# Performance work log

Hardware: AMD Instinct MI355X
Metric: run time of the kernel (lower is better)

## Reference

```python
import jax, jax.numpy as jnp
import numpy as np

B, CIN, COUT, HID, L, H, W = 4, 3, 1, 128, 4, 256, 256


def setup_inputs() -> dict:
    key = jax.random.key(0)
    ks = jax.random.split(key, 12)
    u = 1.0 / (HID * HID)
    inp = {
        "x": jax.random.normal(ks[0], (B, CIN, H, W), dtype=jnp.float32),
        "lin_in_w": jax.random.normal(ks[1], (CIN, HID), dtype=jnp.float32) * 0.1,
        "lin_in_b": jnp.zeros((HID,), dtype=jnp.float32),
        "wr": jax.random.uniform(ks[2], (L, HID, HID), dtype=jnp.float32) * u,
        "wi": jax.random.uniform(ks[3], (L, HID, HID), dtype=jnp.float32) * u,
        "br": jax.random.normal(ks[4], (L, HID), dtype=jnp.float32) * 0.01,
        "bi": jax.random.normal(ks[5], (L, HID), dtype=jnp.float32) * 0.01,
        "cw": jax.random.normal(ks[6], (L, HID, HID), dtype=jnp.float32) * (1.0 / np.sqrt(HID)),
        "cb": jnp.zeros((L, HID), dtype=jnp.float32),
        "lin_out_w": jax.random.normal(ks[7], (HID, COUT), dtype=jnp.float32) * 0.1,
        "lin_out_b": jnp.zeros((COUT,), dtype=jnp.float32),
    }
    return inp


def _gelu(x):
    return jax.nn.gelu(x, approximate=False)  # torch F.gelu default = exact erf


def _spectral_conv(x, wr, wi, br, bi):
    # x: (B, C, H, W) -> rfft2 over last two dims, per-frequency channel mix
    sp = jnp.fft.rfft2(x, axes=(-2, -1))  # (B, C, H, W//2+1) complex
    re = jnp.einsum('bixy,io->boxy', sp.real, wr) + br[None, :, None, None]
    im = jnp.einsum('bixy,io->boxy', sp.imag, wi) + bi[None, :, None, None]
    return jnp.fft.irfft2(re + 1j * im, s=x.shape[-2:], axes=(-2, -1))


def reference(x, lin_in_w, lin_in_b, wr, wi, br, bi, cw, cb, lin_out_w, lin_out_b):
    # input transform: BCHW -> BHWC -> Linear -> gelu -> BCHW
    h = jnp.einsum('bchw,cd->bdhw', x, lin_in_w) + lin_in_b[None, :, None, None]
    h = _gelu(h)
    for l in range(L):
        spatial = jnp.einsum('bihw,oi->bohw', h, cw[l]) + cb[l][None, :, None, None]  # 1x1 conv
        h = _gelu(spatial + _spectral_conv(h, wr[l], wi[l], br[l], bi[l]))
    # output transform
    y = jnp.einsum('bchw,cd->bdhw', h, lin_out_w) + lin_out_b[None, :, None, None]
    return _gelu(y)
```

## Files before the change

### kernel.cpp

```cpp
#include <hip/hip_runtime.h>

#define W2_FLOATS   131072
#define RB_FLOATS   131072
#define WBF_USHORTS 262144

typedef short s8v __attribute__((ext_vector_type(8)));
typedef float f4v __attribute__((ext_vector_type(4)));
typedef float f2v __attribute__((ext_vector_type(2)));

#if defined(__has_builtin)
#  if __has_builtin(__builtin_amdgcn_cvt_pk_bf16_f32)
#    define HAVE_PK_BF16 1
#  endif
#endif
#ifndef HAVE_PK_BF16
#  define HAVE_PK_BF16 0
#endif

__device__ __forceinline__ unsigned short bf16_rne(float v) {
    unsigned u = __float_as_uint(v);
    unsigned r = u + 0x7FFFu + ((u >> 16) & 1u);
    return (unsigned short)(r >> 16);
}
__device__ __forceinline__ float bf16_tof(unsigned short x) {
    return __uint_as_float(((unsigned)x) << 16);
}
__device__ __forceinline__ unsigned pk_bf16(float a, float b) {
#if HAVE_PK_BF16
    typedef __bf16 bf16x2 __attribute__((ext_vector_type(2)));
    bf16x2 v = __builtin_amdgcn_cvt_pk_bf16_f32(a, b);
    return __builtin_bit_cast(unsigned, v);
#else
    return (unsigned)bf16_rne(a) | ((unsigned)bf16_rne(b) << 16);
#endif
}

__device__ __forceinline__ float gelu_f(float x) {
    float ax = fabsf(x);
    float z  = ax * 0.7071067811865476f;
    float t  = __builtin_amdgcn_rcpf(fmaf(0.3275911f, z, 1.0f));
    float p  = t * fmaf(t, fmaf(t, fmaf(t, fmaf(t, 1.061405429f, -1.453152027f),
                                        1.421413741f), -0.284496736f), 0.254829592f);
    float e  = __expf(-z * z);
    float hx = 0.5f * ax;
    return fmaf(0.5f, x, hx) - hx * p * e;
}
__device__ __forceinline__ f2v gelu2(f2v x) {
    f2v ax; ax.x = fabsf(x.x); ax.y = fabsf(x.y);
    f2v z   = ax * 0.7071067811865476f;
    f2v den = z * 0.3275911f + 1.0f;
    f2v t;  t.x = __builtin_amdgcn_rcpf(den.x); t.y = __builtin_amdgcn_rcpf(den.y);
    f2v p = t * (t * (t * (t * (t * 1.061405429f + (-1.453152027f)) + 1.421413741f)
              + (-0.284496736f)) + 0.254829592f);
    f2v nz2 = -z * z;
    f2v e;  e.x = __expf(nz2.x); e.y = __expf(nz2.y);
    f2v hx = ax * 0.5f;
    return (x * 0.5f + hx) - (hx * p) * e;
}

__global__ void prep_all(const float* __restrict__ wr, const float* __restrict__ wi,
                         const float* __restrict__ cw,
                         const float* __restrict__ br, const float* __restrict__ bi,
                         float* __restrict__ W2, unsigned short* __restrict__ Wbf,
                         float* __restrict__ RB) {
    int bid = blockIdx.x;
    if (bid < 512) {
        int idx = bid * 256 + threadIdx.x;
        {
            int l = idx >> 15, which = (idx >> 14) & 1, i = (idx >> 7) & 127, o = idx & 127;
            const float* w = which ? wi : wr;
            W2[idx] = 0.5f * (cw[(l << 14) + (o << 7) + i] + w[(l << 14) + (i << 7) + o]);
        }
        {
            int t = idx;
            int j = t & 7, col = (t >> 3) & 127, quad = (t >> 10) & 3;
            int m2 = (t >> 12) & 1, kc = (t >> 13) & 3, l = t >> 15;
            int k = kc * 32 + quad * 8 + j;
            const float* w = m2 ? wi : wr;
            float v = 0.5f * (cw[(l << 14) + (col << 7) + k] + w[(l << 14) + (k << 7) + col]);
            unsigned short hi = bf16_rne(v);
            unsigned short lo = bf16_rne(v - bf16_tof(hi));
            int base = (l * 4 + kc) * 16384;
            Wbf[base + (((m2 * 2 + 0) * 4 + quad) * 128 + col) * 8 + j] = hi;
            Wbf[base + (((m2 * 2 + 1) * 4 + quad) * 128 + col) * 8 + j] = lo;
        }
    } else {
        int idx = (bid - 512) * 256 + threadIdx.x;
        int l = idx >> 15, c = (idx >> 7) & 255, o = idx & 127;
        float v;
        if (c == 0) {
            v = br[(l << 7) + o];
        } else {
            float s = 0.0f;
            for (int k = 1; k < 128; k++) {
                int m = (k * c) & 255;
                s += sinf(0.024543692952156857f * (float)m);
            }
            v = -bi[(l << 7) + o] * s * 0.0078125f;
        }
        RB[idx] = v;
    }
}

#define APAD 40
#define A_IDX(sd, kt, hf, pair, qj) ((((((sd)*4 + (kt))*2 + (hf))*32 + (pair))*APAD) + (qj))
#define W_IDX(m2, hf, quad, col) (((((m2)*2 + (hf))*4 + (quad))*128 + (col))*8)

__device__ __forceinline__ void layer_core(const unsigned short* Abuf,
        const unsigned short* __restrict__ Wl, int wv, int l15, int quad,
        f4v U[2], f4v V[2])
{
    U[0] = (f4v){0.f, 0.f, 0.f, 0.f}; U[1] = (f4v){0.f, 0.f, 0.f, 0.f};
    V[0] = (f4v){0.f, 0.f, 0.f, 0.f}; V[1] = (f4v){0.f, 0.f, 0.f, 0.f};
    #pragma unroll
    for (int kc = 0; kc < 4; kc++) {
        {
            s8v b0 = *(const s8v*)&Wl[kc * 16384 + W_IDX(0, 0, quad, wv * 16 + l15)];
            s8v b1 = *(const s8v*)&Wl[kc * 16384 + W_IDX(0, 1, quad, wv * 16 + l15)];
            s8v ah0 = *(const s8v*)&Abuf[A_IDX(0, kc, 0, l15,      quad * 8)];
            s8v ah1 = *(const s8v*)&Abuf[A_IDX(0, kc, 0, 16 + l15, quad * 8)];
            s8v al0 = *(const s8v*)&Abuf[A_IDX(0, kc, 1, l15,      quad * 8)];
            s8v al1 = *(const s8v*)&Abuf[A_IDX(0, kc, 1, 16 + l15, quad * 8)];
            U[0] = __builtin_amdgcn_mfma_f32_16x16x32_bf16(ah0, b0, U[0], 0, 0, 0);
            U[1] = __builtin_amdgcn_mfma_f32_16x16x32_bf16(ah1, b0, U[1], 0, 0, 0);
            U[0] = __builtin_amdgcn_mfma_f32_16x16x32_bf16(ah0, b1, U[0], 0, 0, 0);
            U[1] = __builtin_amdgcn_mfma_f32_16x16x32_bf16(ah1, b1, U[1], 0, 0, 0);
            U[0] = __builtin_amdgcn_mfma_f32_16x16x32_bf16(al0, b0, U[0], 0, 0, 0);
            U[1] = __builtin_amdgcn_mfma_f32_16x16x32_bf16(al1, b0, U[1], 0, 0, 0);
        }
        {
            s8v b0 = *(const s8v*)&Wl[kc * 16384 + W_IDX(1, 0, quad, wv * 16 + l15)];
            s8v b1 = *(const s8v*)&Wl[kc * 16384 + W_IDX(1, 1, quad, wv * 16 + l15)];
            s8v ah0 = *(const s8v*)&Abuf[A_IDX(1, kc, 0, l15,      quad * 8)];
            s8v ah1 = *(const s8v*)&Abuf[A_IDX(1, kc, 0, 16 + l15, quad * 8)];
            s8v al0 = *(const s8v*)&Abuf[A_IDX(1, kc, 1, l15,      quad * 8)];
            s8v al1 = *(const s8v*)&Abuf[A_IDX(1, kc, 1, 16 + l15, quad * 8)];
            V[0] = __builtin_amdgcn_mfma_f32_16x16x32_bf16(ah0, b0, V[0], 0, 0, 0);
            V[1] = __builtin_amdgcn_mfma_f32_16x16x32_bf16(ah1, b0, V[1], 0, 0, 0);
            V[0] = __builtin_amdgcn_mfma_f32_16x16x32_bf16(ah0, b1, V[0], 0, 0, 0);
            V[1] = __builtin_amdgcn_mfma_f32_16x16x32_bf16(ah1, b1, V[1], 0, 0, 0);
            V[0] = __builtin_amdgcn_mfma_f32_16x16x32_bf16(al0, b0, V[0], 0, 0, 0);
            V[1] = __builtin_amdgcn_mfma_f32_16x16x32_bf16(al1, b0, V[1], 0, 0, 0);
        }
    }
}

__global__ __launch_bounds__(512, 6) void fno_fused(
        const float* __restrict__ x,
        const float* __restrict__ w_in, const float* __restrict__ b_in,
        const unsigned short* __restrict__ Wbf,
        const float* __restrict__ W2,
        const float* __restrict__ RB,
        const float* __restrict__ cb,
        const float* __restrict__ wo, const float* __restrict__ bo,
        float* __restrict__ out)
{
    __shared__ unsigned short Abuf[2 * 4 * 2 * 32 * APAD];

    int bid = blockIdx.x;
    int tid = threadIdx.x;

    if (bid >= 4096) {
        float* Hs = (float*)Abuf;
        int b2 = bid - 4096;
        int o = tid & 127;
        int rowp = (tid < 128) ? 0 : 128;
        float hval = 0.0f;
        if (tid < 256) {
            float acc = b_in[o];
            #pragma unroll
            for (int c = 0; c < 3; c++)
                acc = fmaf(x[((b2 * 3 + c) << 16) + (rowp << 8)], w_in[c * 128 + o], acc);
            hval = gelu_f(acc);
        }
        for (int l = 0; l < 4; l++) {
            __syncthreads();
            if (tid < 256) Hs[tid] = hval;
            __syncthreads();
            if (tid < 256) {
                const float* W2l = W2 + l * 32768;
                const float* hb = Hs + ((tid < 128) ? 0 : 128);
                float a2 = 0.0f;
                for (int i = 0; i < 128; i++) a2 = fmaf(W2l[(i << 7) + o], hb[i], a2);
                a2 = 2.0f * a2 + cb[l * 128 + o];
                if (tid < 128) a2 += RB[l * 32768 + o];
                hval = gelu_f(a2);
            }
        }
        __syncthreads();
        if (tid < 256) Hs[tid] = hval * wo[o];
        __syncthreads();
        #pragma unroll
        for (int off = 64; off >= 1; off >>= 1) {
            if (tid < 256 && (tid & 127) < off) Hs[tid] += Hs[tid + off];
            __syncthreads();
        }
        if (tid < 256 && (tid & 127) == 0) out[(b2 << 16) + (rowp << 8)] = gelu_f(Hs[tid] + bo[0]);
        return;
    }

    int b = bid >> 10;
    int rem = bid & 1023;
    int r, c0, rq;
    bool rowzero;
    if (rem < 1016) {
        r = 1 + (rem >> 3);
        c0 = (rem & 7) << 5;
        rq = 256 - r;
        rowzero = false;
    } else {
        int idx2 = rem - 1016;
        r = (idx2 < 4) ? 0 : 128;
        c0 = 1 + ((idx2 & 3) << 5);
        rq = r;
        rowzero = (r == 0);
    }

    {
        int j2 = tid >> 4;
        int seg = tid & 15;
        int ch0 = seg << 3;
        int cp = c0 + j2;
        int cq = (256 - cp) & 255;
        float xp[3], xq[3];
        #pragma unroll
        for (int c = 0; c < 3; c++) {
            xp[c] = x[((b * 3 + c) << 16) + (r << 8) + cp];
            xq[c] = x[((b * 3 + c) << 16) + (rq << 8) + cq];
        }
        int kt = seg >> 2;
        int qj = (seg & 3) << 3;
        alignas(16) unsigned short sh[8], sl[8], dh[8], dl[8];
        #pragma unroll
        for (int jj = 0; jj < 8; jj++) {
            int d = ch0 + jj;
            float bv = b_in[d];
            f2v acc2; acc2.x = bv; acc2.y = bv;
            #pragma unroll
            for (int c = 0; c < 3; c++) {
                float w = w_in[c * 128 + d];
                f2v xv; xv.x = xp[c]; xv.y = xq[c];
                acc2 = xv * w + acc2;
            }
            f2v g = gelu2(acc2);
            float s = g.x + g.y, dd = g.x - g.y;
            unsigned hpk = pk_bf16(s, dd);
            f2v res;
            res.x = s  - __uint_as_float(hpk << 16);
            res.y = dd - __uint_as_float(hpk & 0xFFFF0000u);
            unsigned lpk = pk_bf16(res.x, res.y);
            sh[jj] = (unsigned short)hpk; dh[jj] = (unsigned short)(hpk >> 16);
            sl[jj] = (unsigned short)lpk; dl[jj] = (unsigned short)(lpk >> 16);
        }
        *(s8v*)&Abuf[A_IDX(0, kt, 0, j2, qj)] = *(const s8v*)sh;
        *(s8v*)&Abuf[A_IDX(0, kt, 1, j2, qj)] = *(const s8v*)sl;
        *(s8v*)&Abuf[A_IDX(1, kt, 0, j2, qj)] = *(const s8v*)dh;
        *(s8v*)&Abuf[A_IDX(1, kt, 1, j2, qj)] = *(const s8v*)dl;
    }

    int lane = tid & 63;
    int wv = tid >> 6;
    int l15 = lane & 15;
    int quad = lane >> 4;
    int och = wv * 16 + l15;
    int rkt = wv >> 1;
    int rqj = ((wv & 1) << 4) + l15;

    for (int l = 0; l < 3; l++) {
        __syncthreads();
        f4v U[2], V[2];
        layer_core(Abuf, Wbf + l * 65536, wv, l15, quad, U, V);
        __syncthreads();

        const float* RBl = RB + l * 32768;
        float cbv = cb[l * 128 + och];
        #pragma unroll
        for (int mt = 0; mt < 2; mt++)
            #pragma unroll
            for (int rg = 0; rg < 4; rg++) {
                int pair = mt * 16 + quad * 4 + rg;
                int colp = c0 + pair;
                int colq = (256 - colp) & 255;
                float u = U[mt][rg], v = V[mt][rg];
                f2v bpq; bpq.x = u + v + cbv; bpq.y = u - v + cbv;
                if (rowzero) {
                    bpq.x += RBl[(colp << 7) + och];
                    bpq.y += RBl[(colq << 7) + och];
                }
                f2v g = gelu2(bpq);
                float s = g.x + g.y, dd = g.x - g.y;
                unsigned hpk = pk_bf16(s, dd);
                f2v res;
                res.x = s  - __uint_as_float(hpk << 16);
                res.y = dd - __uint_as_float(hpk & 0xFFFF0000u);
                unsigned lpk = pk_bf16(res.x, res.y);
                Abuf[A_IDX(0, rkt, 0, pair, rqj)] = (unsigned short)hpk;
                Abuf[A_IDX(1, rkt, 0, pair, rqj)] = (unsigned short)(hpk >> 16);
                Abuf[A_IDX(0, rkt, 1, pair, rqj)] = (unsigned short)lpk;
                Abuf[A_IDX(1, rkt, 1, pair, rqj)] = (unsigned short)(lpk >> 16);
            }
    }

    float pp[8], pq[8];
    {
        __syncthreads();
        f4v U[2], V[2];
        layer_core(Abuf, Wbf + 3 * 65536, wv, l15, quad, U, V);
        __syncthreads();

        float wov = wo[och];
        const float* RBl = RB + 3 * 32768;
        float cbv = cb[3 * 128 + och];
        #pragma unroll
        for (int mt = 0; mt < 2; mt++)
            #pragma unroll
            for (int rg = 0; rg < 4; rg++) {
                int pair = mt * 16 + quad * 4 + rg;
                int colp = c0 + pair;
                int colq = (256 - colp) & 255;
                float u = U[mt][rg], v = V[mt][rg];
                f2v bpq; bpq.x = u + v + cbv; bpq.y = u - v + cbv;
                if (rowzero) {
                    bpq.x += RBl[(colp << 7) + och];
                    bpq.y += RBl[(colq << 7) + och];
                }
                f2v g = gelu2(bpq);
                pp[mt * 4 + rg] = g.x * wov;
                pq[mt * 4 + rg] = g.y * wov;
            }
    }

    #pragma unroll
    for (int i = 0; i < 8; i++) {
        #pragma unroll
        for (int m = 1; m <= 8; m <<= 1) {
            pp[i] += __shfl_xor(pp[i], m, 64);
            pq[i] += __shfl_xor(pq[i], m, 64);
        }
    }
    float* Pb = (float*)Abuf;
    if (l15 == 0) {
        #pragma unroll
        for (int mt = 0; mt < 2; mt++)
            #pragma unroll
            for (int rg = 0; rg < 4; rg++) {
                int pair = mt * 16 + quad * 4 + rg;
                Pb[(pair << 3) + wv]        = pp[mt * 4 + rg];
                Pb[256 + (pair << 3) + wv]  = pq[mt * 4 + rg];
            }
    }
    __syncthreads();
    if (tid < 64) {
        int pqsel = tid >> 5;
        int pair = tid & 31;
        const float* pb = Pb + pqsel * 256 + (pair << 3);
        float ssum = ((pb[0] + pb[1]) + (pb[2] + pb[3])) +
                     ((pb[4] + pb[5]) + (pb[6] + pb[7])) + bo[0];
        int colp = c0 + pair;
        int col = pqsel ? ((256 - colp) & 255) : colp;
        int row = pqsel ? rq : r;
        out[(b << 16) + (row << 8) + col] = gelu_f(ssum);
    }
}

extern "C" void kernel_launch(void* const* d_in, const int* in_sizes, int n_in,
                              void* d_out, int out_size, void* d_ws, size_t ws_size,
                              hipStream_t stream) {
    const float* x         = (const float*)d_in[0];
    const float* lin_in_w  = (const float*)d_in[1];
    const float* lin_in_b  = (const float*)d_in[2];
    const float* wr        = (const float*)d_in[3];
    const float* wi        = (const float*)d_in[4];
    const float* br        = (const float*)d_in[5];
    const float* bi        = (const float*)d_in[6];
    const float* cw        = (const float*)d_in[7];
    const float* cb        = (const float*)d_in[8];
    const float* lin_out_w = (const float*)d_in[9];
    const float* lin_out_b = (const float*)d_in[10];
    float* out = (float*)d_out;

    size_t need = (size_t)(W2_FLOATS + RB_FLOATS) * sizeof(float)
                + (size_t)WBF_USHORTS * sizeof(unsigned short);
    if (ws_size < need) return;
    float* ws = (float*)d_ws;
    float* W2 = ws;
    float* RB = W2 + W2_FLOATS;
    unsigned short* Wbf = (unsigned short*)(RB + RB_FLOATS);

    prep_all<<<1024, 256, 0, stream>>>(wr, wi, cw, br, bi, W2, Wbf, RB);
    fno_fused<<<4100, 512, 0, stream>>>(x, lin_in_w, lin_in_b, Wbf, W2, RB,
                                        cb, lin_out_w, lin_out_b, out);
}
```

Measured before the change: 327.9 us.

## Halve block tile to 16 columns, 256 threads, each wave covering 32 output channels

Retiles the fused FNO kernel so each block handles 16 column pairs instead of 32, using 4 waves of 256 threads where each wave computes 32 output channels (two N tiles) rather than 16. Shared memory per block halves and the grid doubles to 8196 blocks. Inside a wave, A fragments are now reused across two B tiles instead of B being reused across two A tiles. The intent is higher occupancy and better latency hiding from smaller blocks. The cost is twice as many blocks, each issuing its own weight loads from global memory, plus more per-block overhead.

Result: slower. 385.7 us (median of 2 runs) (+17.6%).

```diff
diff --git a/kernel.cpp b/kernel.cpp
--- a/kernel.cpp
+++ b/kernel.cpp
@@ -103,7 +103,7 @@
 }
 
 #define APAD 40
-#define A_IDX(sd, kt, hf, pair, qj) ((((((sd)*4 + (kt))*2 + (hf))*32 + (pair))*APAD) + (qj))
+#define A_IDX(sd, kt, hf, pair, qj) ((((((sd)*4 + (kt))*2 + (hf))*16 + (pair))*APAD) + (qj))
 #define W_IDX(m2, hf, quad, col) (((((m2)*2 + (hf))*4 + (quad))*128 + (col))*8)
 
 __device__ __forceinline__ void layer_core(const unsigned short* Abuf,
@@ -112,40 +112,41 @@
 {
     U[0] = (f4v){0.f, 0.f, 0.f, 0.f}; U[1] = (f4v){0.f, 0.f, 0.f, 0.f};
     V[0] = (f4v){0.f, 0.f, 0.f, 0.f}; V[1] = (f4v){0.f, 0.f, 0.f, 0.f};
+    int colbase = (wv << 5) + l15;
     #pragma unroll
     for (int kc = 0; kc < 4; kc++) {
         {
-            s8v b0 = *(const s8v*)&Wl[kc * 16384 + W_IDX(0, 0, quad, wv * 16 + l15)];
-            s8v b1 = *(const s8v*)&Wl[kc * 16384 + W_IDX(0, 1, quad, wv * 16 + l15)];
-            s8v ah0 = *(const s8v*)&Abuf[A_IDX(0, kc, 0, l15,      quad * 8)];
-            s8v ah1 = *(const s8v*)&Abuf[A_IDX(0, kc, 0, 16 + l15, quad * 8)];
-            s8v al0 = *(const s8v*)&Abuf[A_IDX(0, kc, 1, l15,      quad * 8)];
-            s8v al1 = *(const s8v*)&Abuf[A_IDX(0, kc, 1, 16 + l15, quad * 8)];
-            U[0] = __builtin_amdgcn_mfma_f32_16x16x32_bf16(ah0, b0, U[0], 0, 0, 0);
-            U[1] = __builtin_amdgcn_mfma_f32_16x16x32_bf16(ah1, b0, U[1], 0, 0, 0);
-            U[0] = __builtin_amdgcn_mfma_f32_16x16x32_bf16(ah0, b1, U[0], 0, 0, 0);
-            U[1] = __builtin_amdgcn_mfma_f32_16x16x32_bf16(ah1, b1, U[1], 0, 0, 0);
-            U[0] = __builtin_amdgcn_mfma_f32_16x16x32_bf16(al0, b0, U[0], 0, 0, 0);
-            U[1] = __builtin_amdgcn_mfma_f32_16x16x32_bf16(al1, b0, U[1], 0, 0, 0);
+            s8v b00 = *(const s8v*)&Wl[kc * 16384 + W_IDX(0, 0, quad, colbase)];
+            s8v b01 = *(const s8v*)&Wl[kc * 16384 + W_IDX(0, 0, quad, colbase + 16)];
+            s8v b10 = *(const s8v*)&Wl[kc * 16384 + W_IDX(0, 1, quad, colbase)];
+            s8v b11 = *(const s8v*)&Wl[kc * 16384 + W_IDX(0, 1, quad, colbase + 16)];
+            s8v ah = *(const s8v*)&Abuf[A_IDX(0, kc, 0, l15, quad * 8)];
+            s8v al = *(const s8v*)&Abuf[A_IDX(0, kc, 1, l15, quad * 8)];
+            U[0] = __builtin_amdgcn_mfma_f32_16x16x32_bf16(ah, b00, U[0], 0, 0, 0);
+            U[1] = __builtin_amdgcn_mfma_f32_16x16x32_bf16(ah, b01, U[1], 0, 0, 0);
+            U[0] = __builtin_amdgcn_mfma_f32_16x16x32_bf16(ah, b10, U[0], 0, 0, 0);
+            U[1] = __builtin_amdgcn_mfma_f32_16x16x32_bf16(ah, b11, U[1], 0, 0, 0);
+            U[0] = __builtin_amdgcn_mfma_f32_16x16x32_bf16(al, b00, U[0], 0, 0, 0);
+            U[1] = __builtin_amdgcn_mfma_f32_16x16x32_bf16(al, b01, U[1], 0, 0, 0);
         }
         {
-            s8v b0 = *(const s8v*)&Wl[kc * 16384 + W_IDX(1, 0, quad, wv * 16 + l15)];
-            s8v b1 = *(const s8v*)&Wl[kc * 16384 + W_IDX(1, 1, quad, wv * 16 + l15)];
-            s8v ah0 = *(const s8v*)&Abuf[A_IDX(1, kc, 0, l15,      quad * 8)];
-            s8v ah1 = *(const s8v*)&Abuf[A_IDX(1, kc, 0, 16 + l15, quad * 8)];
-            s8v al0 = *(const s8v*)&Abuf[A_IDX(1, kc, 1, l15,      quad * 8)];
-            s8v al1 = *(const s8v*)&Abuf[A_IDX(1, kc, 1, 16 + l15, quad * 8)];
-            V[0] = __builtin_amdgcn_mfma_f32_16x16x32_bf16(ah0, b0, V[0], 0, 0, 0);
-            V[1] = __builtin_amdgcn_mfma_f32_16x16x32_bf16(ah1, b0, V[1], 0, 0, 0);
-            V[0] = __builtin_amdgcn_mfma_f32_16x16x32_bf16(ah0, b1, V[0], 0, 0, 0);
-            V[1] = __builtin_amdgcn_mfma_f32_16x16x32_bf16(ah1, b1, V[1], 0, 0, 0);
-            V[0] = __builtin_amdgcn_mfma_f32_16x16x32_bf16(al0, b0, V[0], 0, 0, 0);
-            V[1] = __builtin_amdgcn_mfma_f32_16x16x32_bf16(al1, b0, V[1], 0, 0, 0);
-        }
-    }
-}
-
-__global__ __launch_bounds__(512, 6) void fno_fused(
+            s8v b00 = *(const s8v*)&Wl[kc * 16384 + W_IDX(1, 0, quad, colbase)];
+            s8v b01 = *(const s8v*)&Wl[kc * 16384 + W_IDX(1, 0, quad, colbase + 16)];
+            s8v b10 = *(const s8v*)&Wl[kc * 16384 + W_IDX(1, 1, quad, colbase)];
+            s8v b11 = *(const s8v*)&Wl[kc * 16384 + W_IDX(1, 1, quad, colbase + 16)];
+            s8v ah = *(const s8v*)&Abuf[A_IDX(1, kc, 0, l15, quad * 8)];
+            s8v al = *(const s8v*)&Abuf[A_IDX(1, kc, 1, l15, quad * 8)];
+            V[0] = __builtin_amdgcn_mfma_f32_16x16x32_bf16(ah, b00, V[0], 0, 0, 0);
+            V[1] = __builtin_amdgcn_mfma_f32_16x16x32_bf16(ah, b01, V[1], 0, 0, 0);
+            V[0] = __builtin_amdgcn_mfma_f32_16x16x32_bf16(ah, b10, V[0], 0, 0, 0);
+            V[1] = __builtin_amdgcn_mfma_f32_16x16x32_bf16(ah, b11, V[1], 0, 0, 0);
+            V[0] = __builtin_amdgcn_mfma_f32_16x16x32_bf16(al, b00, V[0], 0, 0, 0);
+            V[1] = __builtin_amdgcn_mfma_f32_16x16x32_bf16(al, b01, V[1], 0, 0, 0);
+        }
+    }
+}
+
+__global__ __launch_bounds__(256, 6) void fno_fused(
         const float* __restrict__ x,
         const float* __restrict__ w_in, const float* __restrict__ b_in,
         const unsigned short* __restrict__ Wbf,
@@ -155,63 +156,58 @@
         const float* __restrict__ wo, const float* __restrict__ bo,
         float* __restrict__ out)
 {
-    __shared__ unsigned short Abuf[2 * 4 * 2 * 32 * APAD];
+    __shared__ unsigned short Abuf[2 * 4 * 2 * 16 * APAD];
 
     int bid = blockIdx.x;
     int tid = threadIdx.x;
 
-    if (bid >= 4096) {
+    if (bid >= 8192) {
         float* Hs = (float*)Abuf;
-        int b2 = bid - 4096;
+        int b2 = bid - 8192;
         int o = tid & 127;
         int rowp = (tid < 128) ? 0 : 128;
-        float hval = 0.0f;
-        if (tid < 256) {
-            float acc = b_in[o];
-            #pragma unroll
-            for (int c = 0; c < 3; c++)
-                acc = fmaf(x[((b2 * 3 + c) << 16) + (rowp << 8)], w_in[c * 128 + o], acc);
-            hval = gelu_f(acc);
-        }
+        float acc = b_in[o];
+        #pragma unroll
+        for (int c = 0; c < 3; c++)
+            acc = fmaf(x[((b2 * 3 + c) << 16) + (rowp << 8)], w_in[c * 128 + o], acc);
+        float hval = gelu_f(acc);
         for (int l = 0; l < 4; l++) {
             __syncthreads();
-            if (tid < 256) Hs[tid] = hval;
+            Hs[tid] = hval;
             __syncthreads();
-            if (tid < 256) {
-                const float* W2l = W2 + l * 32768;
-                const float* hb = Hs + ((tid < 128) ? 0 : 128);
-                float a2 = 0.0f;
-                for (int i = 0; i < 128; i++) a2 = fmaf(W2l[(i << 7) + o], hb[i], a2);
-                a2 = 2.0f * a2 + cb[l * 128 + o];
-                if (tid < 128) a2 += RB[l * 32768 + o];
-                hval = gelu_f(a2);
-            }
-        }
-        __syncthreads();
-        if (tid < 256) Hs[tid] = hval * wo[o];
+            const float* W2l = W2 + l * 32768;
+            const float* hb = Hs + ((tid < 128) ? 0 : 128);
+            float a2 = 0.0f;
+            for (int i = 0; i < 128; i++) a2 = fmaf(W2l[(i << 7) + o], hb[i], a2);
+            a2 = 2.0f * a2 + cb[l * 128 + o];
+            if (tid < 128) a2 += RB[l * 32768 + o];
+            hval = gelu_f(a2);
+        }
+        __syncthreads();
+        Hs[tid] = hval * wo[o];
         __syncthreads();
         #pragma unroll
         for (int off = 64; off >= 1; off >>= 1) {
-            if (tid < 256 && (tid & 127) < off) Hs[tid] += Hs[tid + off];
+            if ((tid & 127) < off) Hs[tid] += Hs[tid + off];
             __syncthreads();
         }
-        if (tid < 256 && (tid & 127) == 0) out[(b2 << 16) + (rowp << 8)] = gelu_f(Hs[tid] + bo[0]);
+        if ((tid & 127) == 0) out[(b2 << 16) + (rowp << 8)] = gelu_f(Hs[tid] + bo[0]);
         return;
     }
 
-    int b = bid >> 10;
-    int rem = bid & 1023;
+    int b = bid >> 11;
+    int rem = bid & 2047;
     int r, c0, rq;
     bool rowzero;
-    if (rem < 1016) {
-        r = 1 + (rem >> 3);
-        c0 = (rem & 7) << 5;
+    if (rem < 2032) {
+        r = 1 + (rem >> 4);
+        c0 = (rem & 15) << 4;
         rq = 256 - r;
         rowzero = false;
     } else {
-        int idx2 = rem - 1016;
-        r = (idx2 < 4) ? 0 : 128;
-        c0 = 1 + ((idx2 & 3) << 5);
+        int idx2 = rem - 2032;
+        r = (idx2 < 8) ? 0 : 128;
+        c0 = 1 + ((idx2 & 7) << 4);
         rq = r;
         rowzero = (r == 0);
     }
@@ -262,9 +258,8 @@
     int wv = tid >> 6;
     int l15 = lane & 15;
     int quad = lane >> 4;
-    int och = wv * 16 + l15;
-    int rkt = wv >> 1;
-    int rqj = ((wv & 1) << 4) + l15;
+    int och0 = (wv << 5) + l15;
+    int och1 = och0 + 16;
 
     for (int l = 0; l < 3; l++) {
         __syncthreads();
@@ -273,15 +268,17 @@
         __syncthreads();
 
         const float* RBl = RB + l * 32768;
-        float cbv = cb[l * 128 + och];
-        #pragma unroll
-        for (int mt = 0; mt < 2; mt++)
+        #pragma unroll
+        for (int nt = 0; nt < 2; nt++) {
+            int och = nt ? och1 : och0;
+            float cbv = cb[l * 128 + och];
+            int rqj = (nt << 4) + l15;
             #pragma unroll
             for (int rg = 0; rg < 4; rg++) {
-                int pair = mt * 16 + quad * 4 + rg;
+                int pair = quad * 4 + rg;
                 int colp = c0 + pair;
                 int colq = (256 - colp) & 255;
-                float u = U[mt][rg], v = V[mt][rg];
+                float u = U[nt][rg], v = V[nt][rg];
                 f2v bpq; bpq.x = u + v + cbv; bpq.y = u - v + cbv;
                 if (rowzero) {
                     bpq.x += RBl[(colp << 7) + och];
@@ -294,44 +291,49 @@
                 res.x = s  - __uint_as_float(hpk << 16);
                 res.y = dd - __uint_as_float(hpk & 0xFFFF0000u);
                 unsigned lpk = pk_bf16(res.x, res.y);
-                Abuf[A_IDX(0, rkt, 0, pair, rqj)] = (unsigned short)hpk;
-                Abuf[A_IDX(1, rkt, 0, pair, rqj)] = (unsigned short)(hpk >> 16);
-                Abuf[A_IDX(0, rkt, 1, pair, rqj)] = (unsigned short)lpk;
-                Abuf[A_IDX(1, rkt, 1, pair, rqj)] = (unsigned short)(lpk >> 16);
+                Abuf[A_IDX(0, wv, 0, pair, rqj)] = (unsigned short)hpk;
+                Abuf[A_IDX(1, wv, 0, pair, rqj)] = (unsigned short)(hpk >> 16);
+                Abuf[A_IDX(0, wv, 1, pair, rqj)] = (unsigned short)lpk;
+                Abuf[A_IDX(1, wv, 1, pair, rqj)] = (unsigned short)(lpk >> 16);
             }
-    }
-
-    float pp[8], pq[8];
+        }
+    }
+
+    float pp[4], pq[4];
     {
         __syncthreads();
         f4v U[2], V[2];
         layer_core(Abuf, Wbf + 3 * 65536, wv, l15, quad, U, V);
         __syncthreads();
 
-        float wov = wo[och];
         const float* RBl = RB + 3 * 32768;
-        float cbv = cb[3 * 128 + och];
-        #pragma unroll
-        for (int mt = 0; mt < 2; mt++)
+        #pragma unroll
+        for (int i = 0; i < 4; i++) { pp[i] = 0.0f; pq[i] = 0.0f; }
+        #pragma unroll
+        for (int nt = 0; nt < 2; nt++) {
+            int och = nt ? och1 : och0;
+            float cbv = cb[3 * 128 + och];
+            float wov = wo[och];
             #pragma unroll
             for (int rg = 0; rg < 4; rg++) {
-                int pair = mt * 16 + quad * 4 + rg;
+                int pair = quad * 4 + rg;
                 int colp = c0 + pair;
                 int colq = (256 - colp) & 255;
-                float u = U[mt][rg], v = V[mt][rg];
+                float u = U[nt][rg], v = V[nt][rg];
                 f2v bpq; bpq.x = u + v + cbv; bpq.y = u - v + cbv;
                 if (rowzero) {
                     bpq.x += RBl[(colp << 7) + och];
                     bpq.y += RBl[(colq << 7) + och];
                 }
                 f2v g = gelu2(bpq);
-                pp[mt * 4 + rg] = g.x * wov;
-                pq[mt * 4 + rg] = g.y * wov;
+                pp[rg] = fmaf(g.x, wov, pp[rg]);
+                pq[rg] = fmaf(g.y, wov, pq[rg]);
             }
+        }
     }
 
     #pragma unroll
-    for (int i = 0; i < 8; i++) {
+    for (int i = 0; i < 4; i++) {
         #pragma unroll
         for (int m = 1; m <= 8; m <<= 1) {
             pp[i] += __shfl_xor(pp[i], m, 64);
@@ -341,21 +343,18 @@
     float* Pb = (float*)Abuf;
     if (l15 == 0) {
         #pragma unroll
-        for (int mt = 0; mt < 2; mt++)
-            #pragma unroll
-            for (int rg = 0; rg < 4; rg++) {
-                int pair = mt * 16 + quad * 4 + rg;
-                Pb[(pair << 3) + wv]        = pp[mt * 4 + rg];
-                Pb[256 + (pair << 3) + wv]  = pq[mt * 4 + rg];
-            }
+        for (int rg = 0; rg < 4; rg++) {
+            int pair = quad * 4 + rg;
+            Pb[(pair << 2) + wv]       = pp[rg];
+            Pb[64 + (pair << 2) + wv]  = pq[rg];
+        }
     }
     __syncthreads();
-    if (tid < 64) {
-        int pqsel = tid >> 5;
-        int pair = tid & 31;
-        const float* pb = Pb + pqsel * 256 + (pair << 3);
-        float ssum = ((pb[0] + pb[1]) + (pb[2] + pb[3])) +
-                     ((pb[4] + pb[5]) + (pb[6] + pb[7])) + bo[0];
+    if (tid < 32) {
+        int pqsel = tid >> 4;
+        int pair = tid & 15;
+        const float* pb = Pb + pqsel * 64 + (pair << 2);
+        float ssum = (pb[0] + pb[1]) + (pb[2] + pb[3]) + bo[0];
         int colp = c0 + pair;
         int col = pqsel ? ((256 - colp) & 255) : colp;
         int row = pqsel ? rq : r;
@@ -388,6 +387,6 @@
     unsigned short* Wbf = (unsigned short*)(RB + RB_FLOATS);
 
     prep_all<<<1024, 256, 0, stream>>>(wr, wi, cw, br, bi, W2, Wbf, RB);
-    fno_fused<<<4100, 512, 0, stream>>>(x, lin_in_w, lin_in_b, Wbf, W2, RB,
+    fno_fused<<<8196, 256, 0, stream>>>(x, lin_in_w, lin_in_b, Wbf, W2, RB,
                                         cb, lin_out_w, lin_out_b, out);
 }
```
